# Kernel tuning notes

Hardware: AMD Instinct MI355X
Metric: run time of the kernel (lower is better)

The kernel has to match this reference:

```python
import jax, jax.numpy as jnp
import numpy as np

# Model dims (match init_kwargs)
N, IN_CH, EMB_CH, CONV_CH, NUM_HEAD, ORIG_DIM, DEG = 256, 64, 64, 128, 2, 64, 16
C2 = CONV_CH // 2          # GAT hidden dim
NEG_SLOPE = 0.2            # PyG GATv2 default leaky_relu slope
E_TOTAL = N * DEG + N      # random edges + self loops (add_self_loops=True default)


def setup_inputs() -> dict:
    key = jax.random.key(0)
    ks = jax.random.split(key, 32)

    def p(k, shape):
        # xavier-ish: scale by 1/sqrt(fan_in)
        return jax.random.normal(k, shape, jnp.float32) / np.float32(np.sqrt(shape[0]))

    x = jax.random.normal(ks[0], (N, IN_CH), jnp.float32)
    E_emb = jax.random.normal(ks[1], (N, EMB_CH), jnp.float32)
    # random graph + self loops (PyG GATv2Conv adds self loops by default)
    src = jax.random.randint(ks[2], (N * DEG,), 0, N, jnp.int32)
    dst = jax.random.randint(ks[3], (N * DEG,), 0, N, jnp.int32)
    loops = jnp.arange(N, dtype=jnp.int32)
    edge_index = jnp.stack([jnp.concatenate([src, loops]),
                            jnp.concatenate([dst, loops])])  # [2, E_TOTAL]

    inp = {
        "x": x,
        "E_emb": E_emb,
        "edge_index": edge_index,
        "node_proj": p(ks[4], (IN_CH, CONV_CH)),
        "emb_proj": p(ks[5], (EMB_CH, CONV_CH)),
        # Conv1d(conv_ch, conv_ch, k=2, s=2) on a length-2 signal == two matmuls
        "conv_w0": p(ks[6], (CONV_CH, CONV_CH)),   # applied to E channel (stack pos 0)
        "conv_w1": p(ks[7], (CONV_CH, CONV_CH)),   # applied to masked x (stack pos 1)
        "conv_b": jnp.zeros((CONV_CH,), jnp.float32),
        "lin2_w": p(ks[8], (CONV_CH, C2)),
        "lin2_b": jnp.zeros((C2,), jnp.float32),
        "masked_proj": p(ks[9], (C2, C2)),
        "normal_proj": p(ks[10], (C2, C2)),
        # GATv2 layer 1
        "g1_wl": p(ks[11], (C2, NUM_HEAD * C2)), "g1_bl": jnp.zeros((NUM_HEAD * C2,), jnp.float32),
        "g1_wr": p(ks[12], (C2, NUM_HEAD * C2)), "g1_br": jnp.zeros((NUM_HEAD * C2,), jnp.float32),
        "g1_att": p(ks[13], (NUM_HEAD, C2)), "g1_bias": jnp.zeros((C2,), jnp.float32),
        # GATv2 layer 2
        "g2_wl": p(ks[14], (C2, NUM_HEAD * C2)), "g2_bl": jnp.zeros((NUM_HEAD * C2,), jnp.float32),
        "g2_wr": p(ks[15], (C2, NUM_HEAD * C2)), "g2_br": jnp.zeros((NUM_HEAD * C2,), jnp.float32),
        "g2_att": p(ks[16], (NUM_HEAD, C2)), "g2_bias": jnp.zeros((C2,), jnp.float32),
        "rec_w": p(ks[17], (C2, ORIG_DIM)),
        "rec_b": jnp.zeros((ORIG_DIM,), jnp.float32),
    }
    return inp


def _forward(x, E_emb, edge_index,
             node_proj, emb_proj, conv_w0, conv_w1, conv_b, lin2_w, lin2_b,
             masked_proj, normal_proj,
             g1_wl, g1_bl, g1_wr, g1_br, g1_att, g1_bias,
             g2_wl, g2_bl, g2_wr, g2_br, g2_att, g2_bias,
             rec_w, rec_b):
    n = x.shape[0]
    src, dst = edge_index[0], edge_index[1]

    x_p = x @ node_proj          # [N, CONV_CH]
    E_p = E_emb @ emb_proj       # [N, CONV_CH]
    # conv1d(k=2,s=2) over stacked [E_p, masked_x] -> base is the unmasked result
    x_w1 = x_p @ conv_w1                          # per-row contribution of x
    base = E_p @ conv_w0 + x_w1 + conv_b          # [N, CONV_CH]

    def gatv2(h, wl, bl, wr, br, att, bias):
        # PyG GATv2Conv, concat=False (head mean), negative_slope=0.2, eval mode
        xl = (h @ wl + bl).reshape(n, NUM_HEAD, C2)   # source transform
        xr = (h @ wr + br).reshape(n, NUM_HEAD, C2)   # target transform
        e = jax.nn.leaky_relu(xl[src] + xr[dst], NEG_SLOPE)   # [E, H, C2]
        logit = jnp.einsum('ehc,hc->eh', e, att)              # [E, H]
        mx = jax.ops.segment_max(logit, dst, num_segments=n)  # per-target max
        w = jnp.exp(logit - mx[dst])
        denom = jax.ops.segment_sum(w, dst, num_segments=n)
        alpha = w / (denom[dst] + 1e-16)
        out = jax.ops.segment_sum(xl[src] * alpha[:, :, None], dst, num_segments=n)
        return out.mean(axis=1) + bias                        # [N, C2]

    def per_node(i):
        # masking row i of x_p zeroes its contribution to the conv output
        h = jnp.tanh(base.at[i].add(-x_w1[i]))
        m = h @ lin2_w + lin2_b                               # [N, C2]
        proj = m @ normal_proj
        proj = proj.at[i].set(m[i] @ masked_proj)
        g = jax.nn.elu(gatv2(proj, g1_wl, g1_bl, g1_wr, g1_br, g1_att, g1_bias))
        g = jax.nn.elu(gatv2(g, g2_wl, g2_bl, g2_wr, g2_br, g2_att, g2_bias))
        return g[i] @ rec_w + rec_b                           # only row i is used

    recon = jax.vmap(per_node)(jnp.arange(n))                 # [N, ORIG_DIM]
    return jnp.tanh(recon)


def reference(x, E_emb, edge_index,
              node_proj, emb_proj, conv_w0, conv_w1, conv_b, lin2_w, lin2_b,
              masked_proj, normal_proj,
              g1_wl, g1_bl, g1_wr, g1_br, g1_att, g1_bias,
              g2_wl, g2_bl, g2_wr, g2_br, g2_att, g2_bias,
              rec_w, rec_b):
    return _forward(x, E_emb, edge_index,
                    node_proj, emb_proj, conv_w0, conv_w1, conv_b, lin2_w, lin2_b,
                    masked_proj, normal_proj,
                    g1_wl, g1_bl, g1_wr, g1_br, g1_att, g1_bias,
                    g2_wl, g2_bl, g2_wr, g2_br, g2_att, g2_bias,
                    rec_w, rec_b)
```

## Files before the change

kernel.cpp:

```cpp
#include <hip/hip_runtime.h>
#include <hip/hip_bf16.h>


#define NN 256
#define EDGE_CAP 96
#define E2_CAP 64
#define E_CAP 6144
#define M_CAP 8

#define OFF_G1ATT  115136
#define OFF_G1BIAS 115264
#define OFF_G2WL   115328
#define OFF_G2BL   123520
#define OFF_G2WR   123648
#define OFF_G2BR   131840
#define OFF_G2ATT  131968
#define OFF_G2BIAS 132096
#define OFF_RECW   132160
#define OFF_RECB   136256
#define W_TOTAL    136320

__device__ float g_w[W_TOTAL];
__device__ __align__(16) float g_xl0[NN*128];
__device__ __align__(16) float g_xr0[NN*128];
__device__ __align__(16) float g_xlV[NN*128];
__device__ __align__(16) float g_xrV[NN*128];
__device__ __align__(16) float g_xl2_0[NN*128];
__device__ __align__(16) float g_num[NN*128];
__device__ float g_m[NN*2], g_den[NN*2];
__device__ float g_elog[E_CAP*2];
__device__ int   g_in_ptr[NN+1], g_out_ptr[NN+1];
__device__ int   g_in_src[E_CAP], g_out_dst[E_CAP];
__device__ int   g_f32;

typedef const void* cvp;
typedef unsigned short ushort8v __attribute__((ext_vector_type(8)));

__device__ __forceinline__ float b2f(__hip_bfloat16 v) { return __bfloat162float(v); }
__device__ __forceinline__ float bfbits(unsigned short u) {
  union { unsigned int i; float f; } c; c.i = ((unsigned int)u) << 16; return c.f;
}

template<typename T> __device__ __forceinline__ float ldv(cvp p, int i);
template<> __device__ __forceinline__ float ldv<float>(cvp p, int i) {
  return ((const float*)p)[i];
}
template<> __device__ __forceinline__ float ldv<__hip_bfloat16>(cvp p, int i) {
  return b2f(((const __hip_bfloat16*)p)[i]);
}

template<typename T>
__device__ __forceinline__ void stage8k(float* dst, cvp src, int elemOff, int t)
{
  if constexpr (sizeof(T) == 4) {
    const float4* s = (const float4*)((const float*)src + elemOff);
    float4* d = (float4*)dst;
    #pragma unroll
    for (int r = 0; r < 8; ++r) d[r*256 + t] = s[r*256 + t];
  } else {
    const ushort8v* s = (const ushort8v*)((const __hip_bfloat16*)src + elemOff);
    #pragma unroll
    for (int r = 0; r < 4; ++r) {
      const ushort8v v = s[r*256 + t];
      float4* d = (float4*)(dst + (r*256 + t)*8);
      float4 lo, hi;
      lo.x = bfbits(v[0]); lo.y = bfbits(v[1]); lo.z = bfbits(v[2]); lo.w = bfbits(v[3]);
      hi.x = bfbits(v[4]); hi.y = bfbits(v[5]); hi.z = bfbits(v[6]); hi.w = bfbits(v[7]);
      d[0] = lo; d[1] = hi;
    }
  }
}

template<typename T>
__device__ __forceinline__ void stage4k(float* dst, cvp src, int t)
{
  if constexpr (sizeof(T) == 4) {
    const float4* s = (const float4*)src;
    float4* d = (float4*)dst;
    #pragma unroll
    for (int r = 0; r < 4; ++r) d[r*256 + t] = s[r*256 + t];
  } else {
    const ushort8v* s = (const ushort8v*)src;
    #pragma unroll
    for (int r = 0; r < 2; ++r) {
      const ushort8v v = s[r*256 + t];
      float4* d = (float4*)(dst + (r*256 + t)*8);
      float4 lo, hi;
      lo.x = bfbits(v[0]); lo.y = bfbits(v[1]); lo.z = bfbits(v[2]); lo.w = bfbits(v[3]);
      hi.x = bfbits(v[4]); hi.y = bfbits(v[5]); hi.z = bfbits(v[6]); hi.w = bfbits(v[7]);
      d[0] = lo; d[1] = hi;
    }
  }
}

struct __align__(16) DenseS {
  float WB[8192];
  float sx[64], sE[64];
  float sxp[128], sEp[128];
  float sA[128];
  float scb[128], sl2b[64], sbl[128], sbr[128];
  float sh0[128], shm[128];
  float sm0[64], sMm[64], sp0[64], sV[64];
  float pp[4][128], qq[4][128];
  float pk[4][64], qk[4][64];
};

template<typename T>
__device__ void dense_body(DenseS& S, int j, int t,
    cvp x, cvp E_emb, cvp np, cvp ep, cvp cw0, cvp cw1, cvp cbp,
    cvp l2w, cvp l2bp, cvp mp, cvp npj, cvp wl, cvp blp, cvp wr, cvp brp)
{
  const int c1 = t & 127, kh = t >> 7;
  const int c6 = t & 63,  kg = t >> 6;

  stage8k<T>(S.WB, np, 0, t);
  if (t < 64)        S.sx[t]    = ldv<T>(x,     j*64 + t);
  else if (t < 128)  S.sE[t-64] = ldv<T>(E_emb, j*64 + (t-64));
  __syncthreads();
  { float a = 0.f;
    #pragma unroll
    for (int kk = 0; kk < 32; ++kk) { const int k = kh*32+kk; a += S.sx[k]*S.WB[k*128+c1]; }
    S.pp[kh][c1] = a; }
  __syncthreads();

  stage8k<T>(S.WB, ep, 0, t);
  if (t < 128) S.sxp[t] = S.pp[0][t] + S.pp[1][t];
  __syncthreads();
  { float a = 0.f;
    #pragma unroll
    for (int kk = 0; kk < 32; ++kk) { const int k = kh*32+kk; a += S.sE[k]*S.WB[k*128+c1]; }
    S.qq[kh][c1] = a; }
  __syncthreads();

  stage8k<T>(S.WB, cw1, 0, t);
  if (t < 128) S.sEp[t] = S.qq[0][t] + S.qq[1][t];
  __syncthreads();
  { float a = 0.f;
    #pragma unroll
    for (int kk = 0; kk < 32; ++kk) { const int k = kh*32+kk; a += S.sxp[k]*S.WB[k*128+c1]; }
    S.pp[kh][c1] = a; }
  __syncthreads();

  stage8k<T>(S.WB, cw1, 8192, t);
  __syncthreads();
  { float a = 0.f;
    #pragma unroll
    for (int kk = 0; kk < 32; ++kk) { const int k = kh*32+kk; a += S.sxp[64+k]*S.WB[k*128+c1]; }
    S.pp[2+kh][c1] = a; }
  __syncthreads();

  stage8k<T>(S.WB, cw0, 0, t);
  if (t < 128) S.sA[t] = S.pp[0][t]+S.pp[1][t]+S.pp[2][t]+S.pp[3][t];
  __syncthreads();
  { float a = 0.f;
    #pragma unroll
    for (int kk = 0; kk < 32; ++kk) { const int k = kh*32+kk; a += S.sEp[k]*S.WB[k*128+c1]; }
    S.qq[kh][c1] = a; }
  __syncthreads();

  stage8k<T>(S.WB, cw0, 8192, t);
  if (t < 128) S.scb[t] = ldv<T>(cbp, t);
  __syncthreads();
  { float a = 0.f;
    #pragma unroll
    for (int kk = 0; kk < 32; ++kk) { const int k = kh*32+kk; a += S.sEp[64+k]*S.WB[k*128+c1]; }
    S.qq[2+kh][c1] = a; }
  __syncthreads();

  stage8k<T>(S.WB, l2w, 0, t);
  if (t < 128) {
    const float ew0 = S.qq[0][t]+S.qq[1][t]+S.qq[2][t]+S.qq[3][t];
    S.sh0[t] = tanhf(ew0 + S.sA[t] + S.scb[t]);
    S.shm[t] = tanhf(ew0 + S.scb[t]);
  } else if (t < 192) S.sl2b[t-128] = ldv<T>(l2bp, t-128);
  __syncthreads();
  { float a = 0.f, b = 0.f;
    #pragma unroll
    for (int kk = 0; kk < 32; ++kk) {
      const int k = kg*32+kk; const float w = S.WB[k*64+c6];
      a += S.sh0[k]*w; b += S.shm[k]*w;
    }
    S.pk[kg][c6] = a; S.qk[kg][c6] = b; }
  __syncthreads();

  stage4k<T>(S.WB,        npj, t);
  stage4k<T>(S.WB + 4096, mp,  t);
  if (t < 64) {
    S.sm0[t] = S.sl2b[t] + S.pk[0][t]+S.pk[1][t]+S.pk[2][t]+S.pk[3][t];
    S.sMm[t] = S.sl2b[t] + S.qk[0][t]+S.qk[1][t]+S.qk[2][t]+S.qk[3][t];
  }
  __syncthreads();
  { float a = 0.f, b = 0.f;
    #pragma unroll
    for (int kk = 0; kk < 16; ++kk) {
      const int k = kg*16+kk;
      a += S.sm0[k]*S.WB[k*64+c6];
      b += S.sMm[k]*S.WB[4096 + k*64+c6];
    }
    S.pk[kg][c6] = a; S.qk[kg][c6] = b; }
  __syncthreads();

  stage8k<T>(S.WB, wl, 0, t);
  if (t < 64)       S.sp0[t]    = S.pk[0][t]+S.pk[1][t]+S.pk[2][t]+S.pk[3][t];
  else if (t < 128) S.sV[t-64]  = S.qk[0][t-64]+S.qk[1][t-64]+S.qk[2][t-64]+S.qk[3][t-64];
  else              S.sbl[t-128] = ldv<T>(blp, t-128);
  __syncthreads();
  { float l = 0.f, lv = 0.f;
    #pragma unroll
    for (int kk = 0; kk < 32; ++kk) {
      const int k = kh*32+kk; const float w = S.WB[k*128+c1];
      l += S.sp0[k]*w; lv += S.sV[k]*w;
    }
    S.pp[kh][c1] = l; S.qq[kh][c1] = lv; }
  __syncthreads();

  stage8k<T>(S.WB, wr, 0, t);
  if (t < 128) {
    g_xl0[j*128+t] = S.sbl[t] + S.pp[0][t] + S.pp[1][t];
    g_xlV[j*128+t] = S.sbl[t] + S.qq[0][t] + S.qq[1][t];
  } else S.sbr[t-128] = ldv<T>(brp, t-128);
  __syncthreads();
  { float r = 0.f, rv = 0.f;
    #pragma unroll
    for (int kk = 0; kk < 32; ++kk) {
      const int k = kh*32+kk; const float w = S.WB[k*128+c1];
      r += S.sp0[k]*w; rv += S.sV[k]*w;
    }
    S.pp[kh][c1] = r; S.qq[kh][c1] = rv; }
  __syncthreads();
  if (t < 128) {
    g_xr0[j*128+t] = S.sbr[t] + S.pp[0][t] + S.pp[1][t];
    g_xrV[j*128+t] = S.sbr[t] + S.qq[0][t] + S.qq[1][t];
  }
}

__global__ __launch_bounds__(256) void k_fused(
    cvp x, cvp E_emb, cvp node_proj, cvp emb_proj,
    cvp conv_w0, cvp conv_w1, cvp conv_b, cvp lin2_w, cvp lin2_b,
    cvp masked_proj, cvp normal_proj,
    cvp g1_wl, cvp g1_bl, cvp g1_wr, cvp g1_br, cvp g1_att, cvp g1_bias,
    cvp g2_wl, cvp g2_bl, cvp g2_wr, cvp g2_br, cvp g2_att, cvp g2_bias,
    cvp rec_w, cvp rec_b,
    int n, const int* __restrict__ ei, int E)
{
  const int t = threadIdx.x, b = blockIdx.x;
  __shared__ int s_cnt;
  __shared__ DenseS DS;
  if (t == 0) s_cnt = 0;
  __syncthreads();
  {
    const __hip_bfloat16* xb = (const __hip_bfloat16*)x;
    const int lim = n < 4096 ? n : 4096;
    int c = 0;
    for (int i = t; i < lim; i += 256) {
      const float v = b2f(xb[i]);
      if (!(fabsf(v) <= 16.f)) c++;
    }
    if (c) atomicAdd(&s_cnt, c);
  }
  __syncthreads();
  const int f = (s_cnt > 64) ? 1 : 0;

  if (b < NN) {
    if (f) dense_body<float>(DS, b, t, x, E_emb, node_proj, emb_proj,
                             conv_w0, conv_w1, conv_b, lin2_w, lin2_b,
                             masked_proj, normal_proj, g1_wl, g1_bl, g1_wr, g1_br);
    else   dense_body<__hip_bfloat16>(DS, b, t, x, E_emb, node_proj, emb_proj,
                             conv_w0, conv_w1, conv_b, lin2_w, lin2_b,
                             masked_proj, normal_proj, g1_wl, g1_bl, g1_wr, g1_br);
    return;
  }

  if (t == 0) g_f32 = f;
  {
    cvp segs2[10] = {g1_att, g1_bias, g2_wl, g2_bl, g2_wr, g2_br,
                     g2_att, g2_bias, rec_w, rec_b};
    const int o2[11] = {OFF_G1ATT, OFF_G1BIAS, OFF_G2WL, OFF_G2BL, OFF_G2WR,
                        OFF_G2BR, OFF_G2ATT, OFF_G2BIAS, OFF_RECW, OFF_RECB,
                        W_TOTAL};
    if (f) {
      for (int s = 0; s < 10; ++s) {
        const float* pf = (const float*)segs2[s];
        const int off = o2[s], len = o2[s+1] - off;
        for (int i2 = t; i2 < len; i2 += 256) g_w[off+i2] = pf[i2];
      }
    } else {
      for (int s = 0; s < 10; ++s) {
        const __hip_bfloat16* pb = (const __hip_bfloat16*)segs2[s];
        const int off = o2[s], len = o2[s+1] - off;
        for (int i2 = t; i2 < len; i2 += 256) g_w[off+i2] = b2f(pb[i2]);
      }
    }
  }
  __shared__ int cin[NN], cou[NN], pin[NN], pou[NN];
  if (E > E_CAP) E = E_CAP;
  cin[t] = 0; cou[t] = 0;
  __syncthreads();
  for (int e = t; e < E; e += 256) {
    atomicAdd(&cin[ei[E+e] & (NN-1)], 1);
    atomicAdd(&cou[ei[e]   & (NN-1)], 1);
  }
  __syncthreads();
  pin[t] = cin[t]; pou[t] = cou[t];
  __syncthreads();
  for (int off = 1; off < NN; off <<= 1) {
    int a = 0, c = 0;
    if (t >= off) { a = pin[t-off]; c = pou[t-off]; }
    __syncthreads();
    if (t >= off) { pin[t] += a; pou[t] += c; }
    __syncthreads();
  }
  const int exi = pin[t] - cin[t];
  const int exo = pou[t] - cou[t];
  g_in_ptr[t] = exi; g_out_ptr[t] = exo;
  if (t == NN-1) { g_in_ptr[NN] = pin[t]; g_out_ptr[NN] = pou[t]; }
  cin[t] = exi; cou[t] = exo;
  __syncthreads();
  for (int e = t; e < E; e += 256) {
    const int s = ei[e] & (NN-1), d = ei[E+e] & (NN-1);
    g_in_src[atomicAdd(&cin[d], 1)] = s;
    g_out_dst[atomicAdd(&cou[s], 1)] = d;
  }
}

__global__ __launch_bounds__(256) void k_l1base()
{
  const int j = blockIdx.x, t = threadIdx.x;
  __shared__ __align__(16) float sxr[128];
  __shared__ __align__(16) float satt[128];
  __shared__ float slog[2][EDGE_CAP], sw[2][EDGE_CAP];
  __shared__ float sinv[2], sg1[64], spA[4][64], spB[4][64], sx2[2][128];
  __shared__ int ssrc[EDGE_CAP];
  const int base = g_in_ptr[j];
  int nE = g_in_ptr[j+1] - base;
  if (nE > EDGE_CAP) nE = EDGE_CAP;
  if (t < 128) { sxr[t] = g_xr0[j*128+t]; satt[t] = g_w[OFF_G1ATT + t]; }
  for (int e = t; e < nE; e += 256) ssrc[e] = g_in_src[base+e];
  __syncthreads();
  for (int idx = t; idx < nE*2; idx += 256) {
    const int e = idx >> 1, h = idx & 1, s = ssrc[e];
    const float4* x4 = (const float4*)(g_xl0 + s*128 + h*64);
    const float4* r4 = (const float4*)(sxr + h*64);
    const float4* a4 = (const float4*)(satt + h*64);
    float acc = 0.f;
    #pragma unroll
    for (int q = 0; q < 16; ++q) {
      const float4 xv = x4[q], rv = r4[q], av = a4[q];
      float v0 = xv.x + rv.x; v0 = v0 > 0.f ? v0 : 0.2f*v0;
      float v1 = xv.y + rv.y; v1 = v1 > 0.f ? v1 : 0.2f*v1;
      float v2 = xv.z + rv.z; v2 = v2 > 0.f ? v2 : 0.2f*v2;
      float v3 = xv.w + rv.w; v3 = v3 > 0.f ? v3 : 0.2f*v3;
      acc += av.x*v0 + av.y*v1 + av.z*v2 + av.w*v3;
    }
    slog[h][e] = acc;
    g_elog[(base+e)*2+h] = acc;
  }
  __syncthreads();
  if (t < 128) {
    const int h = t >> 6, lane = t & 63;
    float m = -1e30f;
    for (int e = lane; e < nE; e += 64) m = fmaxf(m, slog[h][e]);
    for (int o = 1; o < 64; o <<= 1) m = fmaxf(m, __shfl_xor(m, o));
    float ssum = 0.f;
    for (int e = lane; e < nE; e += 64) {
      const float w = __expf(slog[h][e]-m); sw[h][e] = w; ssum += w;
    }
    for (int o = 1; o < 64; o <<= 1) ssum += __shfl_xor(ssum, o);
    if (lane == 0) {
      sinv[h] = 1.f/(ssum + 1e-16f);
      g_m[j*2+h] = m; g_den[j*2+h] = ssum;
    }
  }
  __syncthreads();
  {
    const int grp = t >> 6, c = t & 63;
    float a0 = 0.f, a1 = 0.f;
    for (int e = grp; e < nE; e += 4) {
      const float* xs = g_xl0 + ssrc[e]*128;
      a0 += sw[0][e]*xs[c];
      a1 += sw[1][e]*xs[64+c];
    }
    spA[grp][c] = a0; spB[grp][c] = a1;
  }
  __syncthreads();
  if (t < 64) {
    const float a0 = spA[0][t]+spA[1][t]+spA[2][t]+spA[3][t];
    const float a1 = spB[0][t]+spB[1][t]+spB[2][t]+spB[3][t];
    g_num[j*128+t] = a0; g_num[j*128+64+t] = a1;
    float g = 0.5f*(a0*sinv[0] + a1*sinv[1]) + g_w[OFF_G1BIAS + t];
    g = g > 0.f ? g : expm1f(g);
    sg1[t] = g;
  }
  __syncthreads();
  {
    const int c = t & 127, half = t >> 7;
    float acc = 0.f;
    const int k0 = half*32;
    #pragma unroll
    for (int kk = 0; kk < 32; ++kk) {
      const int k = k0 + kk;
      acc += sg1[k]*g_w[OFF_G2WL + k*128+c];
    }
    sx2[half][c] = acc;
  }
  __syncthreads();
  if (t < 128) g_xl2_0[j*128+t] = g_w[OFF_G2BL + t] + sx2[0][t] + sx2[1][t];
}

struct __align__(16) P3s {
  float xl2e[E2_CAP*128];
  float rtmp[M_CAP*128];
  float g1m[M_CAP*64];
  float sgi[64];
  float sxlVi[128], sxl0i[128], sxri[128];
  float satt[128], satt2[128];
  float xr2i[128], sg[64];
  float spE[2][2][64];
  float slog[2][E2_CAP], sw[2][E2_CAP];
  float sinv[2];
  int   slotOf[NN];
  unsigned char isInN[NN];
  int   ssrc2[E2_CAP], listM[M_CAP], listCh[E2_CAP];
  int   nM, nCh;
};

__device__ __forceinline__ void delta_one(P3s& S, int m, int nMl, int i, int t)
{
  if (m >= nMl) return;
  const int lt = t - 128, h = lt >> 6, c = lt & 63;
  const int j = S.listM[m];
  const float mj = g_m[j*2+h];
  float u = S.sxlVi[lt] + g_xr0[j*128+lt];
  u = u > 0.f ? u : 0.2f*u;
  float ln = S.satt[lt]*u;
  for (int o = 1; o < 64; o <<= 1) ln += __shfl_xor(ln, o);
  const float wn1 = __expf(ln - mj);
  const int jb = g_in_ptr[j], jd = g_in_ptr[j+1] - jb;
  float wo = 0.f; int cnt = 0;
  for (int p = c; p < jd; p += 64)
    if (g_in_src[jb+p] == i) { wo += __expf(g_elog[(jb+p)*2+h] - mj); cnt++; }
  for (int o = 1; o < 64; o <<= 1) {
    wo += __shfl_xor(wo, o); cnt += __shfl_xor(cnt, o);
  }
  const float dd = (float)cnt*wn1 - wo;
  const float dn = (float)cnt*wn1*S.sxlVi[lt] - wo*S.sxl0i[lt];
  S.rtmp[m*128+lt] = (g_num[j*128+lt] + dn) / (g_den[j*2+h] + dd + 1e-16f);
}

__global__ __launch_bounds__(256) void k_periter(void* out)
{
  const int i = blockIdx.x, t = threadIdx.x;
  __shared__ P3s S;

  if (t < NN) { S.slotOf[t] = -1; S.isInN[t] = 0; }
  if (t == 0) S.nM = 0;
  if (t < 128) {
    S.satt[t]  = g_w[OFF_G1ATT + t];
    S.satt2[t] = g_w[OFF_G2ATT + t];
    S.sxlVi[t] = g_xlV[i*128+t];
    S.sxl0i[t] = g_xl0[i*128+t];
    S.sxri[t]  = g_xrV[i*128+t];
  }
  __syncthreads();
  if (t == 0) S.slotOf[i] = 0;

  const int b2 = g_in_ptr[i];
  int nE2 = g_in_ptr[i+1] - b2;
  if (nE2 > E2_CAP) nE2 = E2_CAP;
  for (int e = t; e < nE2; e += 256) {
    const int s = g_in_src[b2+e];
    S.ssrc2[e] = s;
    S.isInN[s] = 1;
  }
  __syncthreads();

  const int ob = g_out_ptr[i], onE = g_out_ptr[i+1] - ob;
  for (int e = t; e < onE; e += 256) {
    const int d = g_out_dst[ob+e];
    if (d != i && S.isInN[d]) {
      if (atomicCAS(&S.slotOf[d], -1, -2) == -1) {
        const int p = atomicAdd(&S.nM, 1);
        if (p < M_CAP) { S.listM[p] = d; S.slotOf[d] = p + 1; }
        else S.slotOf[d] = -1;
      }
    }
  }
  for (int idx = t; idx < nE2*2; idx += 256) {
    const int e = idx >> 1, h = idx & 1, s = S.ssrc2[e];
    const float* xls = (s == i) ? (S.sxlVi + h*64) : (g_xl0 + s*128 + h*64);
    const float4* x4 = (const float4*)xls;
    const float4* r4 = (const float4*)(S.sxri + h*64);
    const float4* a4 = (const float4*)(S.satt + h*64);
    float acc = 0.f;
    #pragma unroll
    for (int q = 0; q < 16; ++q) {
      const float4 xv = x4[q], rv = r4[q], av = a4[q];
      float v0 = xv.x + rv.x; v0 = v0 > 0.f ? v0 : 0.2f*v0;
      float v1 = xv.y + rv.y; v1 = v1 > 0.f ? v1 : 0.2f*v1;
      float v2 = xv.z + rv.z; v2 = v2 > 0.f ? v2 : 0.2f*v2;
      float v3 = xv.w + rv.w; v3 = v3 > 0.f ? v3 : 0.2f*v3;
      acc += av.x*v0 + av.y*v1 + av.z*v2 + av.w*v3;
    }
    S.slog[h][e] = acc;
  }
  __syncthreads();
  const int nMl = S.nM > M_CAP ? M_CAP : S.nM;

  if (t < 128) {
    const int h = t >> 6, lane = t & 63;
    float m = -1e30f;
    for (int e = lane; e < nE2; e += 64) m = fmaxf(m, S.slog[h][e]);
    for (int o = 1; o < 64; o <<= 1) m = fmaxf(m, __shfl_xor(m, o));
    float ssum = 0.f;
    for (int e = lane; e < nE2; e += 64) {
      const float w = __expf(S.slog[h][e]-m); S.sw[h][e] = w; ssum += w;
    }
    for (int o = 1; o < 64; o <<= 1) ssum += __shfl_xor(ssum, o);
    if (lane == 0) S.sinv[h] = 1.f/(ssum + 1e-16f);
  } else {
    delta_one(S, 0, nMl, i, t);
  }
  __syncthreads();

  if (t < 128) {
    const int g2 = t >> 6, c = t & 63;
    float a0 = 0.f, a1 = 0.f;
    for (int e = g2; e < nE2; e += 2) {
      const int s = S.ssrc2[e];
      const float* xs = (s == i) ? S.sxlVi : (g_xl0 + s*128);
      a0 += S.sw[0][e]*xs[c];
      a1 += S.sw[1][e]*xs[64+c];
    }
    S.spE[g2][0][c] = a0; S.spE[g2][1][c] = a1;
  } else {
    delta_one(S, 1, nMl, i, t);
  }
  __syncthreads();

  if (t < 64) {
    const float a0 = S.spE[0][0][t] + S.spE[1][0][t];
    const float a1 = S.spE[0][1][t] + S.spE[1][1][t];
    float g = 0.5f*(a0*S.sinv[0] + a1*S.sinv[1]) + g_w[OFF_G1BIAS + t];
    g = g > 0.f ? g : expm1f(g);
    S.sgi[t] = g;
  } else if (t == 64) {
    int nc = 0;
    for (int e = 0; e < nE2; ++e)
      if (S.slotOf[S.ssrc2[e]] >= 0) S.listCh[nc++] = e;
    S.nCh = nc;
  } else if (t >= 128) {
    delta_one(S, 2, nMl, i, t);
  }
  __syncthreads();

  for (int m = 3; m < nMl; ++m) {
    if (t >= 128) delta_one(S, m, nMl, i, t);
    __syncthreads();
  }

  if (t < 128) {
    float v = g_w[OFF_G2BR + t];
    #pragma unroll
    for (int k = 0; k < 64; ++k) v += S.sgi[k]*g_w[OFF_G2WR + k*128+t];
    S.xr2i[t] = v;
  } else {
    for (int idx = t - 128; idx < nMl*64; idx += 128) {
      const int m = idx >> 6, c = idx & 63;
      float g = 0.5f*(S.rtmp[m*128+c] + S.rtmp[m*128+64+c]) + g_w[OFF_G1BIAS + c];
      g = g > 0.f ? g : expm1f(g);
      S.g1m[m*64+c] = g;
    }
  }
  __syncthreads();

  for (int idx = t; idx < nE2*32; idx += 256) {
    const int e = idx >> 5, q = idx & 31;
    ((float4*)S.xl2e)[e*32 + q] =
        *((const float4*)(g_xl2_0 + S.ssrc2[e]*128) + q);
  }
  __syncthreads();
  for (int idx = t; idx < S.nCh*128; idx += 256) {
    const int e = S.listCh[idx >> 7], c = idx & 127;
    const int sl = S.slotOf[S.ssrc2[e]];
    const float* g1r = (sl == 0) ? S.sgi : (S.g1m + (sl-1)*64);
    float v = g_w[OFF_G2BL + c];
    #pragma unroll
    for (int k = 0; k < 64; ++k) v += g1r[k]*g_w[OFF_G2WL + k*128+c];
    S.xl2e[e*128+c] = v;
  }
  __syncthreads();

  for (int idx = t; idx < nE2*2; idx += 256) {
    const int e = idx >> 1, h = idx & 1;
    const float4* x4 = (const float4*)(S.xl2e + e*128 + h*64);
    const float4* r4 = (const float4*)(S.xr2i + h*64);
    const float4* a4 = (const float4*)(S.satt2 + h*64);
    float acc = 0.f;
    #pragma unroll
    for (int q = 0; q < 16; ++q) {
      const float4 xv = x4[q], rv = r4[q], av = a4[q];
      float v0 = xv.x + rv.x; v0 = v0 > 0.f ? v0 : 0.2f*v0;
      float v1 = xv.y + rv.y; v1 = v1 > 0.f ? v1 : 0.2f*v1;
      float v2 = xv.z + rv.z; v2 = v2 > 0.f ? v2 : 0.2f*v2;
      float v3 = xv.w + rv.w; v3 = v3 > 0.f ? v3 : 0.2f*v3;
      acc += av.x*v0 + av.y*v1 + av.z*v2 + av.w*v3;
    }
    S.slog[h][e] = acc;
  }
  __syncthreads();

  if (t < 128) {
    const int h = t >> 6, lane = t & 63;
    float m = -1e30f;
    for (int e = lane; e < nE2; e += 64) m = fmaxf(m, S.slog[h][e]);
    for (int o = 1; o < 64; o <<= 1) m = fmaxf(m, __shfl_xor(m, o));
    float ssum = 0.f;
    for (int e = lane; e < nE2; e += 64) {
      const float w = __expf(S.slog[h][e]-m); S.sw[h][e] = w; ssum += w;
    }
    for (int o = 1; o < 64; o <<= 1) ssum += __shfl_xor(ssum, o);
    if (lane == 0) S.sinv[h] = 1.f/(ssum + 1e-16f);
  }
  __syncthreads();

  if (t < 128) {
    const int g2 = t >> 6, c = t & 63;
    float a0 = 0.f, a1 = 0.f;
    for (int e = g2; e < nE2; e += 2) {
      a0 += S.sw[0][e]*S.xl2e[e*128 + c];
      a1 += S.sw[1][e]*S.xl2e[e*128 + 64 + c];
    }
    S.spE[g2][0][c] = a0; S.spE[g2][1][c] = a1;
  }
  __syncthreads();
  if (t < 64) {
    const float a0 = S.spE[0][0][t] + S.spE[1][0][t];
    const float a1 = S.spE[0][1][t] + S.spE[1][1][t];
    float g = 0.5f*(a0*S.sinv[0] + a1*S.sinv[1]) + g_w[OFF_G2BIAS + t];
    g = g > 0.f ? g : expm1f(g);
    S.sg[t] = g;
  }
  __syncthreads();

  if (t < 64) {
    float v = g_w[OFF_RECB + t];
    #pragma unroll
    for (int c = 0; c < 64; ++c) v += S.sg[c]*g_w[OFF_RECW + c*64+t];
    const float r = tanhf(v);
    if (g_f32) ((float*)out)[i*64+t] = r;
    else       ((__hip_bfloat16*)out)[i*64+t] = __float2bfloat16(r);
  }
}

extern "C" void kernel_launch(void* const* d_in, const int* in_sizes, int n_in,
                              void* d_out, int out_size, void* d_ws, size_t ws_size,
                              hipStream_t stream)
{
  const int* ei = (const int*)d_in[2];
  const int E = in_sizes[2] / 2;

  k_fused<<<NN+1, 256, 0, stream>>>(
      d_in[0], d_in[1], d_in[3], d_in[4], d_in[5], d_in[6], d_in[7],
      d_in[8], d_in[9], d_in[10], d_in[11], d_in[12], d_in[13], d_in[14],
      d_in[15], d_in[16], d_in[17], d_in[18], d_in[19], d_in[20], d_in[21],
      d_in[22], d_in[23], d_in[24], d_in[25],
      in_sizes[0], ei, E);
  k_l1base<<<NN, 256, 0, stream>>>();
  k_periter<<<NN, 256, 0, stream>>>(d_out);
}
```

Measured before the change: 170.8 us.

## Stream bf16 weights into LDS with async global_load_lds and batch dense stages

Adds a bf16-specific dense path that loads raw bf16 weights straight into shared memory using the async global-to-LDS load builtin, issued in a few large bursts instead of per-stage float conversion staging. Matmul phases are merged so fewer barriers are needed, and the left/right GATv2 projections are computed together. The extra block for weight copying and CSR building is removed, with block 0 doing that work after its dense part, and the weight copy is vectorised. This enlarges shared memory use (union of structs, about 96KB of bf16 weights), which may lower occupancy, and serialises the CSR build behind block 0's dense work.

```diff
diff --git a/kernel.cpp b/kernel.cpp
--- a/kernel.cpp
+++ b/kernel.cpp
@@ -20,7 +20,7 @@
 #define OFF_RECB   136256
 #define W_TOTAL    136320
 
-__device__ float g_w[W_TOTAL];
+__device__ __align__(16) float g_w[W_TOTAL];
 __device__ __align__(16) float g_xl0[NN*128];
 __device__ __align__(16) float g_xr0[NN*128];
 __device__ __align__(16) float g_xlV[NN*128];
@@ -49,48 +49,143 @@
   return b2f(((const __hip_bfloat16*)p)[i]);
 }
 
+typedef __attribute__((address_space(1))) void gvoid;
+typedef __attribute__((address_space(3))) void lvoid;
+__device__ __forceinline__ void gld16(const void* g, void* l) {
+  __builtin_amdgcn_global_load_lds((gvoid*)g, (lvoid*)l, 16, 0, 0);
+}
+__device__ __forceinline__ void burst(void* ldsDst, const void* src, int bytes, int t) {
+  const int warp = t >> 6, lane = t & 63;
+  const int nI = bytes >> 10;
+  for (int k = warp; k < nI; k += 4)
+    gld16((const char*)src + k*1024 + lane*16, (char*)ldsDst + k*1024 + lane*16);
+}
+
+struct __align__(16) DenseB {
+  unsigned short U1[32768];
+  unsigned short U2[16384];
+  float sx[64], sE[64];
+  float sxp[128], sEp[128], sA[128];
+  float scb[128], sl2b[64], sbl[128], sbr[128];
+  float sh0[128], shm[128];
+  float sm0[64], sMm[64], sp0[64], sV[64];
+  float pp[2][128], qq[2][128], rr[2][128], ss[2][128];
+  float pk[4][64], qk[4][64];
+};
+
+__device__ void dense_bf16(DenseB& S, int j, int t,
+    cvp x, cvp E_emb, cvp np, cvp ep, cvp cw0, cvp cw1, cvp cbp,
+    cvp l2w, cvp l2bp, cvp mp, cvp npj, cvp wl, cvp blp, cvp wr, cvp brp)
+{
+  const int c1 = t & 127, sel = t >> 7;
+  const int c6 = t & 63,  grp = t >> 6;
+
+  burst(S.U1,          np,  16384, t);
+  burst(S.U1 +  8192,  ep,  16384, t);
+  burst(S.U1 + 16384,  cw1, 32768, t);
+  burst(S.U2,          wl,  16384, t);
+  burst(S.U2 +  8192,  wr,  16384, t);
+  if (t < 128) {
+    S.scb[t] = b2f(((const __hip_bfloat16*)cbp)[t]);
+    S.sbl[t] = b2f(((const __hip_bfloat16*)blp)[t]);
+    S.sbr[t] = b2f(((const __hip_bfloat16*)brp)[t]);
+    if (t < 64) { S.sx[t]   = b2f(((const __hip_bfloat16*)x)[j*64+t]);
+                  S.sl2b[t] = b2f(((const __hip_bfloat16*)l2bp)[t]); }
+    else        S.sE[t-64]  = b2f(((const __hip_bfloat16*)E_emb)[j*64+(t-64)]);
+  }
+  __syncthreads();
+
+  { const unsigned short* W = S.U1 + sel*8192;
+    const float* v = sel ? S.sE : S.sx;
+    float a = 0.f;
+    #pragma unroll
+    for (int k = 0; k < 64; ++k) a += v[k]*bfbits(W[k*128+c1]);
+    if (sel) S.sEp[c1] = a; else S.sxp[c1] = a; }
+  __syncthreads();
+
+  { float a = 0.f;
+    #pragma unroll
+    for (int kk = 0; kk < 64; ++kk) { const int k = sel*64+kk;
+      a += S.sxp[k]*bfbits(S.U1[16384 + k*128+c1]); }
+    S.pp[sel][c1] = a; }
+  __syncthreads();
+
+  burst(S.U1,          cw0, 32768, t);
+  burst(S.U1 + 16384,  l2w, 16384, t);
+  burst(S.U1 + 24576,  npj,  8192, t);
+  burst(S.U1 + 28672,  mp,   8192, t);
+  if (t < 128) S.sA[t] = S.pp[0][t] + S.pp[1][t];
+  __syncthreads();
+
+  { float a = 0.f;
+    #pragma unroll
+    for (int kk = 0; kk < 64; ++kk) { const int k = sel*64+kk;
+      a += S.sEp[k]*bfbits(S.U1[k*128+c1]); }
+    S.qq[sel][c1] = a; }
+  __syncthreads();
+
+  if (t < 128) {
+    const float ew0 = S.qq[0][t] + S.qq[1][t];
+    S.sh0[t] = tanhf(ew0 + S.sA[t] + S.scb[t]);
+    S.shm[t] = tanhf(ew0 + S.scb[t]);
+  }
+  __syncthreads();
+
+  { float a = 0.f, bv = 0.f;
+    #pragma unroll
+    for (int kk = 0; kk < 32; ++kk) { const int k = grp*32+kk;
+      const float w = bfbits(S.U1[16384 + k*64+c6]);
+      a += S.sh0[k]*w; bv += S.shm[k]*w; }
+    S.pk[grp][c6] = a; S.qk[grp][c6] = bv; }
+  __syncthreads();
+  if (t < 64) {
+    S.sm0[t] = S.sl2b[t] + S.pk[0][t]+S.pk[1][t]+S.pk[2][t]+S.pk[3][t];
+    S.sMm[t] = S.sl2b[t] + S.qk[0][t]+S.qk[1][t]+S.qk[2][t]+S.qk[3][t];
+  }
+  __syncthreads();
+
+  { float a = 0.f, bv = 0.f;
+    #pragma unroll
+    for (int kk = 0; kk < 16; ++kk) { const int k = grp*16+kk;
+      a  += S.sm0[k]*bfbits(S.U1[24576 + k*64+c6]);
+      bv += S.sMm[k]*bfbits(S.U1[28672 + k*64+c6]); }
+    S.pk[grp][c6] = a; S.qk[grp][c6] = bv; }
+  __syncthreads();
+  if (t < 64)        S.sp0[t]   = S.pk[0][t]+S.pk[1][t]+S.pk[2][t]+S.pk[3][t];
+  else if (t < 128)  S.sV[t-64] = S.qk[0][t-64]+S.qk[1][t-64]+S.qk[2][t-64]+S.qk[3][t-64];
+  __syncthreads();
+
+  { float l = 0.f, lv = 0.f, r = 0.f, rv = 0.f;
+    #pragma unroll
+    for (int kk = 0; kk < 32; ++kk) { const int k = sel*32+kk;
+      const float a = S.sp0[k], bvv = S.sV[k];
+      const float w0 = bfbits(S.U2[k*128+c1]), w1 = bfbits(S.U2[8192 + k*128+c1]);
+      l += a*w0; lv += bvv*w0; r += a*w1; rv += bvv*w1; }
+    S.pp[sel][c1] = l; S.qq[sel][c1] = lv; S.rr[sel][c1] = r; S.ss[sel][c1] = rv; }
+  __syncthreads();
+  if (t < 128) {
+    g_xl0[j*128+t] = S.sbl[t] + S.pp[0][t] + S.pp[1][t];
+    g_xlV[j*128+t] = S.sbl[t] + S.qq[0][t] + S.qq[1][t];
+    g_xr0[j*128+t] = S.sbr[t] + S.rr[0][t] + S.rr[1][t];
+    g_xrV[j*128+t] = S.sbr[t] + S.ss[0][t] + S.ss[1][t];
+  }
+}
+
 template<typename T>
 __device__ __forceinline__ void stage8k(float* dst, cvp src, int elemOff, int t)
 {
-  if constexpr (sizeof(T) == 4) {
-    const float4* s = (const float4*)((const float*)src + elemOff);
-    float4* d = (float4*)dst;
-    #pragma unroll
-    for (int r = 0; r < 8; ++r) d[r*256 + t] = s[r*256 + t];
-  } else {
-    const ushort8v* s = (const ushort8v*)((const __hip_bfloat16*)src + elemOff);
-    #pragma unroll
-    for (int r = 0; r < 4; ++r) {
-      const ushort8v v = s[r*256 + t];
-      float4* d = (float4*)(dst + (r*256 + t)*8);
-      float4 lo, hi;
-      lo.x = bfbits(v[0]); lo.y = bfbits(v[1]); lo.z = bfbits(v[2]); lo.w = bfbits(v[3]);
-      hi.x = bfbits(v[4]); hi.y = bfbits(v[5]); hi.z = bfbits(v[6]); hi.w = bfbits(v[7]);
-      d[0] = lo; d[1] = hi;
-    }
-  }
-}
-
+  const float4* s = (const float4*)((const float*)src + elemOff);
+  float4* d = (float4*)dst;
+  #pragma unroll
+  for (int r = 0; r < 8; ++r) d[r*256 + t] = s[r*256 + t];
+}
 template<typename T>
 __device__ __forceinline__ void stage4k(float* dst, cvp src, int t)
 {
-  if constexpr (sizeof(T) == 4) {
-    const float4* s = (const float4*)src;
-    float4* d = (float4*)dst;
-    #pragma unroll
-    for (int r = 0; r < 4; ++r) d[r*256 + t] = s[r*256 + t];
-  } else {
-    const ushort8v* s = (const ushort8v*)src;
-    #pragma unroll
-    for (int r = 0; r < 2; ++r) {
-      const ushort8v v = s[r*256 + t];
-      float4* d = (float4*)(dst + (r*256 + t)*8);
-      float4 lo, hi;
-      lo.x = bfbits(v[0]); lo.y = bfbits(v[1]); lo.z = bfbits(v[2]); lo.w = bfbits(v[3]);
-      hi.x = bfbits(v[4]); hi.y = bfbits(v[5]); hi.z = bfbits(v[6]); hi.w = bfbits(v[7]);
-      d[0] = lo; d[1] = hi;
-    }
-  }
+  const float4* s = (const float4*)src;
+  float4* d = (float4*)dst;
+  #pragma unroll
+  for (int r = 0; r < 4; ++r) d[r*256 + t] = s[r*256 + t];
 }
 
 struct __align__(16) DenseS {
@@ -105,17 +200,16 @@
   float pk[4][64], qk[4][64];
 };
 
-template<typename T>
-__device__ void dense_body(DenseS& S, int j, int t,
+__device__ void dense_f32(DenseS& S, int j, int t,
     cvp x, cvp E_emb, cvp np, cvp ep, cvp cw0, cvp cw1, cvp cbp,
     cvp l2w, cvp l2bp, cvp mp, cvp npj, cvp wl, cvp blp, cvp wr, cvp brp)
 {
   const int c1 = t & 127, kh = t >> 7;
   const int c6 = t & 63,  kg = t >> 6;
 
-  stage8k<T>(S.WB, np, 0, t);
-  if (t < 64)        S.sx[t]    = ldv<T>(x,     j*64 + t);
-  else if (t < 128)  S.sE[t-64] = ldv<T>(E_emb, j*64 + (t-64));
+  stage8k<float>(S.WB, np, 0, t);
+  if (t < 64)        S.sx[t]    = ldv<float>(x,     j*64 + t);
+  else if (t < 128)  S.sE[t-64] = ldv<float>(E_emb, j*64 + (t-64));
   __syncthreads();
   { float a = 0.f;
     #pragma unroll
@@ -123,7 +217,7 @@
     S.pp[kh][c1] = a; }
   __syncthreads();
 
-  stage8k<T>(S.WB, ep, 0, t);
+  stage8k<float>(S.WB, ep, 0, t);
   if (t < 128) S.sxp[t] = S.pp[0][t] + S.pp[1][t];
   __syncthreads();
   { float a = 0.f;
@@ -132,7 +226,7 @@
     S.qq[kh][c1] = a; }
   __syncthreads();
 
-  stage8k<T>(S.WB, cw1, 0, t);
+  stage8k<float>(S.WB, cw1, 0, t);
   if (t < 128) S.sEp[t] = S.qq[0][t] + S.qq[1][t];
   __syncthreads();
   { float a = 0.f;
@@ -141,7 +235,7 @@
     S.pp[kh][c1] = a; }
   __syncthreads();
 
-  stage8k<T>(S.WB, cw1, 8192, t);
+  stage8k<float>(S.WB, cw1, 8192, t);
   __syncthreads();
   { float a = 0.f;
     #pragma unroll
@@ -149,7 +243,7 @@
     S.pp[2+kh][c1] = a; }
   __syncthreads();
 
-  stage8k<T>(S.WB, cw0, 0, t);
+  stage8k<float>(S.WB, cw0, 0, t);
   if (t < 128) S.sA[t] = S.pp[0][t]+S.pp[1][t]+S.pp[2][t]+S.pp[3][t];
   __syncthreads();
   { float a = 0.f;
@@ -158,8 +252,8 @@
     S.qq[kh][c1] = a; }
   __syncthreads();
 
-  stage8k<T>(S.WB, cw0, 8192, t);
-  if (t < 128) S.scb[t] = ldv<T>(cbp, t);
+  stage8k<float>(S.WB, cw0, 8192, t);
+  if (t < 128) S.scb[t] = ldv<float>(cbp, t);
   __syncthreads();
   { float a = 0.f;
     #pragma unroll
@@ -167,12 +261,12 @@
     S.qq[2+kh][c1] = a; }
   __syncthreads();
 
-  stage8k<T>(S.WB, l2w, 0, t);
+  stage8k<float>(S.WB, l2w, 0, t);
   if (t < 128) {
     const float ew0 = S.qq[0][t]+S.qq[1][t]+S.qq[2][t]+S.qq[3][t];
     S.sh0[t] = tanhf(ew0 + S.sA[t] + S.scb[t]);
     S.shm[t] = tanhf(ew0 + S.scb[t]);
-  } else if (t < 192) S.sl2b[t-128] = ldv<T>(l2bp, t-128);
+  } else if (t < 192) S.sl2b[t-128] = ldv<float>(l2bp, t-128);
   __syncthreads();
   { float a = 0.f, b = 0.f;
     #pragma unroll
@@ -183,8 +277,8 @@
     S.pk[kg][c6] = a; S.qk[kg][c6] = b; }
   __syncthreads();
 
-  stage4k<T>(S.WB,        npj, t);
-  stage4k<T>(S.WB + 4096, mp,  t);
+  stage4k<float>(S.WB,        npj, t);
+  stage4k<float>(S.WB + 4096, mp,  t);
   if (t < 64) {
     S.sm0[t] = S.sl2b[t] + S.pk[0][t]+S.pk[1][t]+S.pk[2][t]+S.pk[3][t];
     S.sMm[t] = S.sl2b[t] + S.qk[0][t]+S.qk[1][t]+S.qk[2][t]+S.qk[3][t];
@@ -200,10 +294,10 @@
     S.pk[kg][c6] = a; S.qk[kg][c6] = b; }
   __syncthreads();
 
-  stage8k<T>(S.WB, wl, 0, t);
+  stage8k<float>(S.WB, wl, 0, t);
   if (t < 64)       S.sp0[t]    = S.pk[0][t]+S.pk[1][t]+S.pk[2][t]+S.pk[3][t];
   else if (t < 128) S.sV[t-64]  = S.qk[0][t-64]+S.qk[1][t-64]+S.qk[2][t-64]+S.qk[3][t-64];
-  else              S.sbl[t-128] = ldv<T>(blp, t-128);
+  else              S.sbl[t-128] = ldv<float>(blp, t-128);
   __syncthreads();
   { float l = 0.f, lv = 0.f;
     #pragma unroll
@@ -214,11 +308,11 @@
     S.pp[kh][c1] = l; S.qq[kh][c1] = lv; }
   __syncthreads();
 
-  stage8k<T>(S.WB, wr, 0, t);
+  stage8k<float>(S.WB, wr, 0, t);
   if (t < 128) {
     g_xl0[j*128+t] = S.sbl[t] + S.pp[0][t] + S.pp[1][t];
     g_xlV[j*128+t] = S.sbl[t] + S.qq[0][t] + S.qq[1][t];
-  } else S.sbr[t-128] = ldv<T>(brp, t-128);
+  } else S.sbr[t-128] = ldv<float>(brp, t-128);
   __syncthreads();
   { float r = 0.f, rv = 0.f;
     #pragma unroll
@@ -233,6 +327,12 @@
     g_xrV[j*128+t] = S.sbr[t] + S.qq[0][t] + S.qq[1][t];
   }
 }
+
+union SharedU {
+  DenseB nb;
+  DenseS s;
+  struct { int cin[NN], cou[NN], pin[NN], pou[NN]; } csr;
+};
 
 __global__ __launch_bounds__(256) void k_fused(
     cvp x, cvp E_emb, cvp node_proj, cvp emb_proj,
@@ -245,7 +345,7 @@
 {
   const int t = threadIdx.x, b = blockIdx.x;
   __shared__ int s_cnt;
-  __shared__ DenseS DS;
+  __shared__ SharedU SU;
   if (t == 0) s_cnt = 0;
   __syncthreads();
   {
@@ -261,16 +361,15 @@
   __syncthreads();
   const int f = (s_cnt > 64) ? 1 : 0;
 
-  if (b < NN) {
-    if (f) dense_body<float>(DS, b, t, x, E_emb, node_proj, emb_proj,
-                             conv_w0, conv_w1, conv_b, lin2_w, lin2_b,
-                             masked_proj, normal_proj, g1_wl, g1_bl, g1_wr, g1_br);
-    else   dense_body<__hip_bfloat16>(DS, b, t, x, E_emb, node_proj, emb_proj,
-                             conv_w0, conv_w1, conv_b, lin2_w, lin2_b,
-                             masked_proj, normal_proj, g1_wl, g1_bl, g1_wr, g1_br);
-    return;
-  }
-
+  if (f) dense_f32(SU.s, b, t, x, E_emb, node_proj, emb_proj,
+                   conv_w0, conv_w1, conv_b, lin2_w, lin2_b,
+                   masked_proj, normal_proj, g1_wl, g1_bl, g1_wr, g1_br);
+  else   dense_bf16(SU.nb, b, t, x, E_emb, node_proj, emb_proj,
+                   conv_w0, conv_w1, conv_b, lin2_w, lin2_b,
+                   masked_proj, normal_proj, g1_wl, g1_bl, g1_wr, g1_br);
+  if (b != 0) return;
+
+  __syncthreads();
   if (t == 0) g_f32 = f;
   {
     cvp segs2[10] = {g1_att, g1_bias, g2_wl, g2_bl, g2_wr, g2_br,
@@ -280,46 +379,53 @@
                         W_TOTAL};
     if (f) {
       for (int s = 0; s < 10; ++s) {
-        const float* pf = (const float*)segs2[s];
-        const int off = o2[s], len = o2[s+1] - off;
-        for (int i2 = t; i2 < len; i2 += 256) g_w[off+i2] = pf[i2];
+        const float4* pf = (const float4*)segs2[s];
+        const int off = o2[s], len = (o2[s+1] - off) >> 2;
+        for (int i2 = t; i2 < len; i2 += 256)
+          *(float4*)&g_w[off + i2*4] = pf[i2];
       }
     } else {
       for (int s = 0; s < 10; ++s) {
-        const __hip_bfloat16* pb = (const __hip_bfloat16*)segs2[s];
-        const int off = o2[s], len = o2[s+1] - off;
-        for (int i2 = t; i2 < len; i2 += 256) g_w[off+i2] = b2f(pb[i2]);
+        const ushort8v* pb = (const ushort8v*)segs2[s];
+        const int off = o2[s], len = (o2[s+1] - off) >> 3;
+        for (int i2 = t; i2 < len; i2 += 256) {
+          const ushort8v v = pb[i2];
+          float4 lo, hi;
+          lo.x = bfbits(v[0]); lo.y = bfbits(v[1]); lo.z = bfbits(v[2]); lo.w = bfbits(v[3]);
+          hi.x = bfbits(v[4]); hi.y = bfbits(v[5]); hi.z = bfbits(v[6]); hi.w = bfbits(v[7]);
+          *(float4*)&g_w[off + i2*8]     = lo;
+          *(float4*)&g_w[off + i2*8 + 4] = hi;
+        }
       }
     }
   }
-  __shared__ int cin[NN], cou[NN], pin[NN], pou[NN];
   if (E > E_CAP) E = E_CAP;
-  cin[t] = 0; cou[t] = 0;
+  SU.csr.cin[t] = 0; SU.csr.cou[t] = 0;
   __syncthreads();
   for (int e = t; e < E; e += 256) {
-    atomicAdd(&cin[ei[E+e] & (NN-1)], 1);
-    atomicAdd(&cou[ei[e]   & (NN-1)], 1);
-  }
-  __syncthreads();
-  pin[t] = cin[t]; pou[t] = cou[t];
+    atomicAdd(&SU.csr.cin[ei[E+e] & (NN-1)], 1);
+    atomicAdd(&SU.csr.cou[ei[e]   & (NN-1)], 1);
+  }
+  __syncthreads();
+  SU.csr.pin[t] = SU.csr.cin[t]; SU.csr.pou[t] = SU.csr.cou[t];
   __syncthreads();
   for (int off = 1; off < NN; off <<= 1) {
     int a = 0, c = 0;
-    if (t >= off) { a = pin[t-off]; c = pou[t-off]; }
+    if (t >= off) { a = SU.csr.pin[t-off]; c = SU.csr.pou[t-off]; }
     __syncthreads();
-    if (t >= off) { pin[t] += a; pou[t] += c; }
+    if (t >= off) { SU.csr.pin[t] += a; SU.csr.pou[t] += c; }
     __syncthreads();
   }
-  const int exi = pin[t] - cin[t];
-  const int exo = pou[t] - cou[t];
+  const int exi = SU.csr.pin[t] - SU.csr.cin[t];
+  const int exo = SU.csr.pou[t] - SU.csr.cou[t];
   g_in_ptr[t] = exi; g_out_ptr[t] = exo;
-  if (t == NN-1) { g_in_ptr[NN] = pin[t]; g_out_ptr[NN] = pou[t]; }
-  cin[t] = exi; cou[t] = exo;
+  if (t == NN-1) { g_in_ptr[NN] = SU.csr.pin[t]; g_out_ptr[NN] = SU.csr.pou[t]; }
+  SU.csr.cin[t] = exi; SU.csr.cou[t] = exo;
   __syncthreads();
   for (int e = t; e < E; e += 256) {
     const int s = ei[e] & (NN-1), d = ei[E+e] & (NN-1);
-    g_in_src[atomicAdd(&cin[d], 1)] = s;
-    g_out_dst[atomicAdd(&cou[s], 1)] = d;
+    g_in_src[atomicAdd(&SU.csr.cin[d], 1)] = s;
+    g_out_dst[atomicAdd(&SU.csr.cou[s], 1)] = d;
   }
 }
 
@@ -659,7 +765,7 @@
   const int* ei = (const int*)d_in[2];
   const int E = in_sizes[2] / 2;
 
-  k_fused<<<NN+1, 256, 0, stream>>>(
+  k_fused<<<NN, 256, 0, stream>>>(
       d_in[0], d_in[1], d_in[3], d_in[4], d_in[5], d_in[6], d_in[7],
       d_in[8], d_in[9], d_in[10], d_in[11], d_in[12], d_in[13], d_in[14],
       d_in[15], d_in[16], d_in[17], d_in[18], d_in[19], d_in[20], d_in[21],
```

Result: faster. 164.4 us (-3.8%).
